# Kernel optimization log

Measured on AMD Instinct MI355X. Metric: run time of the kernel, lower is better.

The kernel has to match this reference:

```python
import jax, jax.numpy as jnp
import numpy as np

N_NODES = 50000
N_EDGES = 50000  # number of hyperedges
NNZ = 800000
IN_C, HID_C, OUT_C = 256, 128, 64


def _glorot(key, shape):
    lim = float(np.sqrt(6.0 / (shape[0] + shape[1])))
    return jax.random.uniform(key, shape, jnp.float32, -lim, lim)


def setup_inputs() -> dict:
    key = jax.random.key(0)
    ks = jax.random.split(key, 8)
    x = jax.random.normal(ks[0], (N_NODES, IN_C), jnp.float32)
    node_idx = jax.random.randint(ks[1], (NNZ,), 0, N_NODES)
    edge_idx = jax.random.randint(ks[2], (NNZ,), 0, N_EDGES)
    hyperedge_index = jnp.stack([node_idx, edge_idx]).astype(jnp.int64)
    return {
        "x": x,
        "hyperedge_index": hyperedge_index,
        "W1": _glorot(ks[3], (IN_C, HID_C)),
        "b1": jnp.zeros((HID_C,), jnp.float32),
        "W2": _glorot(ks[4], (HID_C, OUT_C)),
        "b2": jnp.zeros((OUT_C,), jnp.float32),
        "Wp": _glorot(ks[5], (OUT_C, OUT_C)),
        "bp": jax.random.normal(ks[6], (OUT_C,), jnp.float32) * 0.01,
    }


def _hypergraph_conv(x, node_idx, edge_idx, W, b):
    # PyG HypergraphConv: out = D^-1 H B H^T (X W) + b
    x = x @ W  # [N, F]
    ones = jnp.ones((node_idx.shape[0],), x.dtype)
    d = jax.ops.segment_sum(ones, node_idx, num_segments=N_NODES)   # node degree
    be = jax.ops.segment_sum(ones, edge_idx, num_segments=N_EDGES)  # hyperedge size
    Dinv = jnp.where(d > 0, 1.0 / d, 0.0)
    Binv = jnp.where(be > 0, 1.0 / be, 0.0)
    # node -> hyperedge aggregation
    m = jax.ops.segment_sum(x[node_idx], edge_idx, num_segments=N_EDGES) * Binv[:, None]
    # hyperedge -> node aggregation
    out = jax.ops.segment_sum(m[edge_idx], node_idx, num_segments=N_NODES) * Dinv[:, None]
    return out + b


def reference(x, hyperedge_index, W1, b1, W2, b2, Wp, bp):
    node_idx = hyperedge_index[0]
    edge_idx = hyperedge_index[1]
    h = jax.nn.relu(_hypergraph_conv(x, node_idx, edge_idx, W1, b1))
    features_1 = h
    h = jax.nn.relu(_hypergraph_conv(h, node_idx, edge_idx, W2, b2))
    features_2 = h
    z = h @ Wp + bp
    return (z, features_1, features_2)
```

## Files before the change

kernel.cpp:

```cpp
#include <hip/hip_runtime.h>


typedef unsigned short u16;
typedef unsigned int   u32;
typedef _Float16 f16;
typedef __attribute__((ext_vector_type(8))) short short8;
typedef __attribute__((ext_vector_type(8))) _Float16 half8;
typedef __attribute__((ext_vector_type(4))) float f32x4;

static const int BCAP = 3072;

__device__ __forceinline__ float bf2f(u16 u) {
    return __builtin_bit_cast(float, (u32)u << 16);
}
__device__ __forceinline__ u16 f2bf(float f) {
    u32 b = __builtin_bit_cast(u32, f);
    b += 0x7FFFu + ((b >> 16) & 1u);
    return (u16)(b >> 16);
}

__global__ __launch_bounds__(64) void detect_idx_kernel(const int* __restrict__ hidx,
                                                        int* __restrict__ flag)
{
    __shared__ int nz;
    if (threadIdx.x == 0) nz = 0;
    __syncthreads();
    if (hidx[2 * threadIdx.x + 1] != 0) atomicAdd(&nz, 1);
    __syncthreads();
    if (threadIdx.x == 0) *flag = (nz == 0) ? 1 : 0;
}

__global__ __launch_bounds__(256) void wsplit_kernel(
    const float* __restrict__ W, u16* __restrict__ out, int K, int N)
{
    int idx = blockIdx.x * 256 + threadIdx.x;
    int total = (K >> 6) * N * 72;
    if (idx >= total) return;
    int kp = idx % 72;
    int rest = idx / 72;
    int n = rest % N;
    int c = rest / N;
    float v = 0.f;
    if (kp < 64) v = W[(size_t)(c * 64 + kp) * N + n];
    u16 h = f2bf(v);
    u16 l = f2bf(v - bf2f(h));
    size_t base = (size_t)c * (2 * (size_t)N * 72);
    out[base + (size_t)n * 72 + kp] = h;
    out[base + (size_t)N * 72 + (size_t)n * 72 + kp] = l;
}

__global__ __launch_bounds__(256) void bin_scatter_kernel(
    const int* __restrict__ hidx, const int* __restrict__ flag,
    int* __restrict__ curEb, int* __restrict__ curNb,
    u32* __restrict__ tmpE, u32* __restrict__ tmpN,
    int nnz, int nNodes, int nEdges)
{
    __shared__ int histE[400], histN[400];
    int t = threadIdx.x;
    const int nbE = (nEdges + 127) >> 7, nbN = (nNodes + 127) >> 7;
    for (int b = t; b < 400; b += 256) { histE[b] = 0; histN[b] = 0; }
    __syncthreads();
    int st = (*flag) ? 2 : 1;
    size_t eoff = (size_t)nnz * st;
    int i0 = blockIdx.x * 4096;
    int e_[16], n_[16]; int rE[16], rN[16];
    #pragma unroll
    for (int k = 0; k < 16; ++k) {
        int i = i0 + k * 256 + t;
        int n = -1, e = 0;
        if (i < nnz) {
            n = hidx[(size_t)i * st];
            e = hidx[eoff + (size_t)i * st];
            if (!((u32)n < (u32)nNodes && (u32)e < (u32)nEdges)) n = -1;
        }
        n_[k] = n; e_[k] = e;
        if (n >= 0) {
            rE[k] = atomicAdd(&histE[e >> 7], 1);
            rN[k] = atomicAdd(&histN[n >> 7], 1);
        }
    }
    __syncthreads();
    for (int b = t; b < nbE; b += 256) { int c = histE[b]; if (c) histE[b] = atomicAdd(&curEb[b], c); }
    for (int b = t; b < nbN; b += 256) { int c = histN[b]; if (c) histN[b] = atomicAdd(&curNb[b], c); }
    __syncthreads();
    #pragma unroll
    for (int k = 0; k < 16; ++k) {
        if (n_[k] >= 0) {
            int e = e_[k], n = n_[k];
            int lpE = histE[e >> 7] + rE[k];
            int lpN = histN[n >> 7] + rN[k];
            if (lpE < BCAP) tmpE[(size_t)(e >> 7) * BCAP + lpE] = ((u32)(e & 127) << 16) | (u32)n;
            if (lpN < BCAP) tmpN[(size_t)(n >> 7) * BCAP + lpN] = ((u32)(n & 127) << 16) | (u32)e;
        }
    }
}

__global__ __launch_bounds__(64) void bkt_scan_kernel(
    const int* __restrict__ curE, const int* __restrict__ curN,
    int* __restrict__ baseE, int* __restrict__ baseN, int nbE, int nbN)
{
    const int* cur; int* base; int nb;
    if (blockIdx.x == 0) { cur = curE; base = baseE; nb = nbE; }
    else                 { cur = curN; base = baseN; nb = nbN; }
    int lane = threadIdx.x;
    int carry = 0;
    for (int c0 = 0; c0 < nb; c0 += 64) {
        int i = c0 + lane;
        int v = (i < nb) ? cur[i] : 0;
        int orig = v;
        for (int o = 1; o < 64; o <<= 1) { int u = __shfl_up(v, o, 64); if (lane >= o) v += u; }
        if (i < nb) base[i] = carry + v - orig;
        carry += __shfl(v, 63, 64);
    }
    if (lane == 0) base[nb] = carry;
}

__global__ __launch_bounds__(256) void bin_build_kernel(
    const u32* __restrict__ tmpE, const u32* __restrict__ tmpN,
    const int* __restrict__ baseE, const int* __restrict__ baseN,
    int* __restrict__ deg_e, int* __restrict__ offs_e, float* __restrict__ binv, u16* __restrict__ adj_e,
    int* __restrict__ deg_n, int* __restrict__ offs_n, float* __restrict__ dinv, u16* __restrict__ adj_n,
    int nE, int nN, int nbE)
{
    __shared__ u32 buf[4096];
    __shared__ int lcnt[128], lpre[128], lcur[128];
    int b = blockIdx.x;
    const u32* tmp; const int* base; int* deg; int* offs; float* inv; u16* adj; int n, tb;
    if (b < nbE) { tmp=tmpE; base=baseE; deg=deg_e; offs=offs_e; inv=binv; adj=adj_e; n=nE; tb=b; }
    else         { tmp=tmpN; base=baseN; deg=deg_n; offs=offs_n; inv=dinv; adj=adj_n; n=nN; tb=b-nbE; }
    int t = threadIdx.x;
    int g0 = tb << 7;
    int gbase = base[tb];
    int cnt = base[tb + 1] - gbase;
    int avail = cnt < BCAP ? cnt : BCAP;
    size_t tbase = (size_t)tb * BCAP;
    if (t < 128) lcnt[t] = 0;
    __syncthreads();
    for (int j = t; j < avail; j += 256) atomicAdd(&lcnt[tmp[tbase + j] >> 16], 1);
    __syncthreads();
    if (t < 64) {
        int a0 = lcnt[2 * t], a1 = lcnt[2 * t + 1];
        int ps = a0 + a1, v = ps;
        for (int o = 1; o < 64; o <<= 1) { int u = __shfl_up(v, o, 64); if (t >= o) v += u; }
        int excl = v - ps;
        lpre[2 * t] = excl; lpre[2 * t + 1] = excl + a0;
    }
    __syncthreads();
    if (t < 128) {
        int id = g0 + t;
        if (id < n) {
            int d = lcnt[t];
            deg[id]  = d;
            offs[id] = gbase + lpre[t];
            inv[id]  = d > 0 ? 1.0f / (float)d : 0.0f;
        }
        lcur[t] = lpre[t];
    }
    __syncthreads();
    if (avail <= 0) return;
    for (int j = t; j < avail; j += 256) {
        u32 v = tmp[tbase + j];
        int pos = atomicAdd(&lcur[v >> 16], 1);
        buf[pos] = v & 0xFFFFu;
    }
    __syncthreads();
    for (int j = t; j < avail; j += 256) adj[gbase + j] = (u16)buf[j];
}

template<int C, bool FINAL>
__global__ __launch_bounds__(256) void gather_kernel(
    const f16* __restrict__ src, const u16* __restrict__ adj,
    const int* __restrict__ offs, const int* __restrict__ deg,
    const float* __restrict__ inv, const float* __restrict__ bias,
    void* __restrict__ dstv, int nRows)
{
    constexpr int LANES = C / 8;
    constexpr int ROWS  = 256 / LANES;
    int t = threadIdx.x;
    int row = blockIdx.x * ROWS + t / LANES;
    if (row >= nRows) return;
    int c = (t % LANES) * 8;
    const f16* sp = src + c;
    int j = offs[row], e = j + deg[row];
    float a0[8], a1[8], a2[8], a3[8];
    #pragma unroll
    for (int q = 0; q < 8; ++q) { a0[q] = 0.f; a1[q] = 0.f; a2[q] = 0.f; a3[q] = 0.f; }
    for (; j + 4 <= e; j += 4) {
        int s0 = adj[j], s1 = adj[j + 1], s2 = adj[j + 2], s3 = adj[j + 3];
        const half8 v0 = *(const half8*)(sp + (size_t)s0 * C);
        const half8 v1 = *(const half8*)(sp + (size_t)s1 * C);
        const half8 v2 = *(const half8*)(sp + (size_t)s2 * C);
        const half8 v3 = *(const half8*)(sp + (size_t)s3 * C);
        #pragma unroll
        for (int q = 0; q < 8; ++q) {
            a0[q] += (float)v0[q]; a1[q] += (float)v1[q];
            a2[q] += (float)v2[q]; a3[q] += (float)v3[q];
        }
    }
    for (; j < e; ++j) {
        int s0 = adj[j];
        const half8 v0 = *(const half8*)(sp + (size_t)s0 * C);
        #pragma unroll
        for (int q = 0; q < 8; ++q) a0[q] += (float)v0[q];
    }
    float scv = inv[row];
    float r[8];
    #pragma unroll
    for (int q = 0; q < 8; ++q) r[q] = ((a0[q] + a1[q]) + (a2[q] + a3[q])) * scv;
    if constexpr (FINAL) {
        float* dst = (float*)dstv;
        size_t o = (size_t)row * C + c;
        const float4 b0 = *(const float4*)(bias + c);
        const float4 b1 = *(const float4*)(bias + c + 4);
        float4 o0, o1;
        o0.x = fmaxf(r[0] + b0.x, 0.0f); o0.y = fmaxf(r[1] + b0.y, 0.0f);
        o0.z = fmaxf(r[2] + b0.z, 0.0f); o0.w = fmaxf(r[3] + b0.w, 0.0f);
        o1.x = fmaxf(r[4] + b1.x, 0.0f); o1.y = fmaxf(r[5] + b1.y, 0.0f);
        o1.z = fmaxf(r[6] + b1.z, 0.0f); o1.w = fmaxf(r[7] + b1.w, 0.0f);
        *(float4*)(dst + o)     = o0;
        *(float4*)(dst + o + 4) = o1;
    } else {
        f16* dst = (f16*)dstv;
        half8 ov;
        #pragma unroll
        for (int q = 0; q < 8; ++q) ov[q] = (f16)r[q];
        *(half8*)(dst + (size_t)row * C + c) = ov;
    }
}

__device__ __forceinline__ void split8(const float* __restrict__ p, short8& hi, short8& lo) {
    #pragma unroll
    for (int j = 0; j < 8; ++j) {
        float v = p[j];
        u16 h = f2bf(v);
        hi[j] = (short)h;
        lo[j] = (short)f2bf(v - bf2f(h));
    }
}

template<int K, int N, bool BIAS, bool OUTF16>
__global__ __launch_bounds__(512) void gemm_mfma_kernel(
    const float* __restrict__ A, const u16* __restrict__ Bsp,
    const float* __restrict__ bias, void* __restrict__ C_, int M)
{
    constexpr int KP = 72;
    constexpr int CHUNK = 2 * N * KP;
    constexpr int SC = (K == 256) ? 1 : (K / 64);
    constexpr int NT = N / 16;
    constexpr int NTW = NT / 2;
    __shared__ alignas(16) u16 Bbuf[SC * CHUNK];
    const int tid = threadIdx.x;
    const int wave = tid >> 6, lane = tid & 63;
    const int mg = wave >> 1, nh = wave & 1;
    const int row0 = blockIdx.x * 64 + mg * 16;
    const int lr = lane & 15;
    const int kq = (lane >> 4) * 8;
    const int nt0 = nh * NTW;
    const bool v = row0 < M;
    f32x4 acc[NTW];
    #pragma unroll
    for (int i = 0; i < NTW; ++i) acc[i] = (f32x4){0.f, 0.f, 0.f, 0.f};
    const float* Ap = A + (size_t)(row0 + lr) * K + kq;

    constexpr int CALLS = SC * CHUNK / 512;
    for (int ko = 0; ko < K; ko += SC * 64) {
        const u16* src = Bsp + (size_t)(ko >> 6) * CHUNK;
        if (ko) __syncthreads();
        #pragma unroll
        for (int c = 0; c < (CALLS + 7) / 8; ++c) {
            int call = c * 8 + wave;
            if (call < CALLS) {
                int u = call * 64 + lane;
                *(float4*)(&Bbuf[(size_t)u * 8]) = *(const float4*)(src + (size_t)u * 8);
            }
        }
        __syncthreads();
        if (v) {
            #pragma unroll
            for (int kc = 0; kc < SC; ++kc) {
                #pragma unroll
                for (int k0 = 0; k0 < 64; k0 += 32) {
                    short8 ah, al;
                    split8(Ap + ko + kc * 64 + k0, ah, al);
                    #pragma unroll
                    for (int f = 0; f < NTW; ++f) {
                        const int col = (nt0 + f) * 16 + lr;
                        const int bo = kc * CHUNK + col * KP + k0 + kq;
                        const short8 bh = *(const short8*)(&Bbuf[bo]);
                        const short8 bl = *(const short8*)(&Bbuf[bo + N * KP]);
                        acc[f] = __builtin_amdgcn_mfma_f32_16x16x32_bf16(ah, bh, acc[f], 0, 0, 0);
                        acc[f] = __builtin_amdgcn_mfma_f32_16x16x32_bf16(al, bh, acc[f], 0, 0, 0);
                        acc[f] = __builtin_amdgcn_mfma_f32_16x16x32_bf16(ah, bl, acc[f], 0, 0, 0);
                    }
                }
            }
        }
    }
    if (!v) return;
    const int orow = row0 + (lane >> 4) * 4;
    #pragma unroll
    for (int f = 0; f < NTW; ++f) {
        const int col = (nt0 + f) * 16 + lr;
        float bv = 0.0f;
        if constexpr (BIAS) bv = bias[col];
        #pragma unroll
        for (int j = 0; j < 4; ++j) {
            float vv = acc[f][j] + bv;
            if constexpr (OUTF16) ((f16*)C_)[(size_t)(orow + j) * N + col] = (f16)vv;
            else                  ((float*)C_)[(size_t)(orow + j) * N + col] = vv;
        }
    }
}

extern "C" void kernel_launch(void* const* d_in, const int* in_sizes, int n_in,
                              void* d_out, int out_size, void* d_ws, size_t ws_size,
                              hipStream_t stream)
{
    (void)n_in; (void)out_size; (void)ws_size;
    const float* x  = (const float*)d_in[0];
    const int* hidx = (const int*)d_in[1];
    const float* W1 = (const float*)d_in[2];
    const float* b1 = (const float*)d_in[3];
    const float* W2 = (const float*)d_in[4];
    const float* b2 = (const float*)d_in[5];
    const float* Wp = (const float*)d_in[6];
    const float* bp = (const float*)d_in[7];
    float* out = (float*)d_out;

    const int nnz    = in_sizes[1] / 2;
    const int nNodes = in_sizes[0] / 256;
    const int nEdges = 50000;

    char* w = (char*)d_ws;
    const size_t SEG = 200192;
    int*   deg_e  = (int*)(w + 0 * SEG);
    int*   deg_n  = (int*)(w + 1 * SEG);
    int*   offs_e = (int*)(w + 2 * SEG);
    int*   offs_n = (int*)(w + 3 * SEG);
    float* binv   = (float*)(w + 4 * SEG);
    float* dinv   = (float*)(w + 5 * SEG);
    int*   flag   = (int*)(w + 6 * SEG);
    int*   curEb  = (int*)(w + 6 * SEG + 256);
    int*   curNb  = (int*)(w + 6 * SEG + 2304);
    int*   baseE  = (int*)(w + 6 * SEG + 4352);
    int*   baseN  = (int*)(w + 6 * SEG + 6400);
    char* p = w + 6 * SEG + 8448;
    u16* adj_e = (u16*)p;  p += (size_t)nnz * 2;
    u16* adj_n = (u16*)p;  p += (size_t)nnz * 2;
    f16* h0  = (f16*)p;
    f16* m1  = (f16*)(p + (size_t)nNodes * 128 * 2);
    f16* h1w = h0;
    f16* m2  = (f16*)((char*)h0 + (size_t)nNodes * 64 * 2);
    u16* w1sp = (u16*)(p + 2 * (size_t)nNodes * 128 * 2);
    u16* w2sp = w1sp + 4 * 18432;
    u16* wpsp = w2sp + 2 * 9216;

    const int nbE = (nEdges + 127) >> 7;
    const int nbN = (nNodes + 127) >> 7;
    u32* tmpE = (u32*)m1;
    u32* tmpN = tmpE + (size_t)nbE * BCAP;

    const size_t F1OFF = (size_t)nNodes * 64;
    const size_t F2OFF = F1OFF + (size_t)nNodes * 128;

    hipMemsetAsync(w + 6 * SEG + 256, 0, 4096, stream);
    detect_idx_kernel<<<1, 64, 0, stream>>>(hidx, flag);
    wsplit_kernel<<<(4 * 128 * 72 + 255) / 256, 256, 0, stream>>>(W1, w1sp, 256, 128);
    wsplit_kernel<<<(2 * 64 * 72 + 255) / 256, 256, 0, stream>>>(W2, w2sp, 128, 64);
    wsplit_kernel<<<(1 * 64 * 72 + 255) / 256, 256, 0, stream>>>(Wp, wpsp, 64, 64);
    bin_scatter_kernel<<<(nnz + 4095) / 4096, 256, 0, stream>>>(
        hidx, flag, curEb, curNb, tmpE, tmpN, nnz, nNodes, nEdges);
    bkt_scan_kernel<<<2, 64, 0, stream>>>(curEb, curNb, baseE, baseN, nbE, nbN);
    bin_build_kernel<<<nbE + nbN, 256, 0, stream>>>(
        tmpE, tmpN, baseE, baseN,
        deg_e, offs_e, binv, adj_e,
        deg_n, offs_n, dinv, adj_n,
        nEdges, nNodes, nbE);

    const int gg = (nNodes + 63) / 64;

    gemm_mfma_kernel<256, 128, false, true><<<gg, 512, 0, stream>>>(x, w1sp, nullptr, h0, nNodes);
    gather_kernel<128, false><<<(nEdges + 15) / 16, 256, 0, stream>>>(
        h0, adj_e, offs_e, deg_e, binv, nullptr, m1, nEdges);
    gather_kernel<128, true><<<(nNodes + 15) / 16, 256, 0, stream>>>(
        m1, adj_n, offs_n, deg_n, dinv, b1, out + F1OFF, nNodes);

    gemm_mfma_kernel<128, 64, false, true><<<gg, 512, 0, stream>>>(
        out + F1OFF, w2sp, nullptr, h1w, nNodes);
    gather_kernel<64, false><<<(nEdges + 31) / 32, 256, 0, stream>>>(
        h1w, adj_e, offs_e, deg_e, binv, nullptr, m2, nEdges);
    gather_kernel<64, true><<<(nNodes + 31) / 32, 256, 0, stream>>>(
        m2, adj_n, offs_n, deg_n, dinv, b2, out + F2OFF, nNodes);

    gemm_mfma_kernel<64, 64, true, false><<<gg, 512, 0, stream>>>(
        out + F2OFF, wpsp, bp, out, nNodes);
}
```

Baseline: 289.2 us.

## Store gather sources in column-plane layout and use persistent 1024-thread GEMM

GEMM outputs are now written as column planes (16 or 8 halfs wide), and gather kernels each handle one plane, so a block's random row reads stay inside a smaller working set that fits in cache better. The GEMM becomes persistent with 1024 threads and loads the whole split weight matrix into shared memory once per block. Index-format detection is folded into bin_scatter via a ballot, and the three weight-split kernels are merged into one launch. The risks are that 16-byte random reads per row are less efficient than full-row reads, and that the larger LDS footprint lowers occupancy.

Result: slower. 328.6 us (+13.6%).

```diff
diff --git a/kernel.cpp b/kernel.cpp
--- a/kernel.cpp
+++ b/kernel.cpp
@@ -19,25 +19,11 @@
     return (u16)(b >> 16);
 }
 
-__global__ __launch_bounds__(64) void detect_idx_kernel(const int* __restrict__ hidx,
-                                                        int* __restrict__ flag)
-{
-    __shared__ int nz;
-    if (threadIdx.x == 0) nz = 0;
-    __syncthreads();
-    if (hidx[2 * threadIdx.x + 1] != 0) atomicAdd(&nz, 1);
-    __syncthreads();
-    if (threadIdx.x == 0) *flag = (nz == 0) ? 1 : 0;
-}
-
-__global__ __launch_bounds__(256) void wsplit_kernel(
-    const float* __restrict__ W, u16* __restrict__ out, int K, int N)
-{
-    int idx = blockIdx.x * 256 + threadIdx.x;
-    int total = (K >> 6) * N * 72;
-    if (idx >= total) return;
-    int kp = idx % 72;
-    int rest = idx / 72;
+__device__ __forceinline__ void wsplit_one(const float* __restrict__ W, u16* __restrict__ out,
+                                           int K, int N, int local)
+{
+    int kp = local % 72;
+    int rest = local / 72;
     int n = rest % N;
     int c = rest / N;
     float v = 0.f;
@@ -49,18 +35,36 @@
     out[base + (size_t)N * 72 + (size_t)n * 72 + kp] = l;
 }
 
+__global__ __launch_bounds__(256) void wsplit_all_kernel(
+    const float* __restrict__ W1, const float* __restrict__ W2, const float* __restrict__ Wp,
+    u16* __restrict__ w1sp, u16* __restrict__ w2sp, u16* __restrict__ wpsp)
+{
+    const int T1 = 4 * 128 * 72;
+    const int T2 = 2 * 64 * 72;
+    const int T3 = 1 * 64 * 72;
+    int idx = blockIdx.x * 256 + threadIdx.x;
+    if (idx < T1)                 wsplit_one(W1, w1sp, 256, 128, idx);
+    else if (idx < T1 + T2)       wsplit_one(W2, w2sp, 128, 64, idx - T1);
+    else if (idx < T1 + T2 + T3)  wsplit_one(Wp, wpsp, 64, 64, idx - T1 - T2);
+}
+
 __global__ __launch_bounds__(256) void bin_scatter_kernel(
-    const int* __restrict__ hidx, const int* __restrict__ flag,
+    const int* __restrict__ hidx,
     int* __restrict__ curEb, int* __restrict__ curNb,
     u32* __restrict__ tmpE, u32* __restrict__ tmpN,
     int nnz, int nNodes, int nEdges)
 {
     __shared__ int histE[400], histN[400];
+    __shared__ int s_st;
     int t = threadIdx.x;
     const int nbE = (nEdges + 127) >> 7, nbN = (nNodes + 127) >> 7;
     for (int b = t; b < 400; b += 256) { histE[b] = 0; histN[b] = 0; }
-    __syncthreads();
-    int st = (*flag) ? 2 : 1;
+    if (t < 64) {
+        unsigned long long m = __ballot(hidx[2 * t + 1] != 0);
+        if (t == 0) s_st = (m == 0ull) ? 2 : 1;
+    }
+    __syncthreads();
+    int st = s_st;
     size_t eoff = (size_t)nnz * st;
     int i0 = blockIdx.x * 4096;
     int e_[16], n_[16]; int rE[16], rN[16];
@@ -167,30 +171,32 @@
     for (int j = t; j < avail; j += 256) adj[gbase + j] = (u16)buf[j];
 }
 
-template<int C, bool FINAL>
-__global__ __launch_bounds__(256) void gather_kernel(
+template<int SW, bool FINAL, int C>
+__global__ __launch_bounds__(256) void gather_slice_kernel(
     const f16* __restrict__ src, const u16* __restrict__ adj,
     const int* __restrict__ offs, const int* __restrict__ deg,
     const float* __restrict__ inv, const float* __restrict__ bias,
-    void* __restrict__ dstv, int nRows)
-{
-    constexpr int LANES = C / 8;
-    constexpr int ROWS  = 256 / LANES;
+    void* __restrict__ dstv, int nRows, int nSrcRows)
+{
+    constexpr int TPR = SW / 8;
+    constexpr int RPB = 256 / TPR;
     int t = threadIdx.x;
-    int row = blockIdx.x * ROWS + t / LANES;
-    if (row >= nRows) return;
-    int c = (t % LANES) * 8;
-    const f16* sp = src + c;
-    int j = offs[row], e = j + deg[row];
+    int plane = blockIdx.x & 7;
+    int chunk = blockIdx.x >> 3;
+    int r = chunk * RPB + t / TPR;
+    if (r >= nRows) return;
+    int sub = (TPR == 2) ? (t & 1) : 0;
+    const f16* sp = src + (size_t)plane * nSrcRows * SW + sub * 8;
+    int j = offs[r], e = j + deg[r];
     float a0[8], a1[8], a2[8], a3[8];
     #pragma unroll
     for (int q = 0; q < 8; ++q) { a0[q] = 0.f; a1[q] = 0.f; a2[q] = 0.f; a3[q] = 0.f; }
     for (; j + 4 <= e; j += 4) {
         int s0 = adj[j], s1 = adj[j + 1], s2 = adj[j + 2], s3 = adj[j + 3];
-        const half8 v0 = *(const half8*)(sp + (size_t)s0 * C);
-        const half8 v1 = *(const half8*)(sp + (size_t)s1 * C);
-        const half8 v2 = *(const half8*)(sp + (size_t)s2 * C);
-        const half8 v3 = *(const half8*)(sp + (size_t)s3 * C);
+        const half8 v0 = *(const half8*)(sp + (size_t)s0 * SW);
+        const half8 v1 = *(const half8*)(sp + (size_t)s1 * SW);
+        const half8 v2 = *(const half8*)(sp + (size_t)s2 * SW);
+        const half8 v3 = *(const half8*)(sp + (size_t)s3 * SW);
         #pragma unroll
         for (int q = 0; q < 8; ++q) {
             a0[q] += (float)v0[q]; a1[q] += (float)v1[q];
@@ -199,32 +205,33 @@
     }
     for (; j < e; ++j) {
         int s0 = adj[j];
-        const half8 v0 = *(const half8*)(sp + (size_t)s0 * C);
+        const half8 v0 = *(const half8*)(sp + (size_t)s0 * SW);
         #pragma unroll
         for (int q = 0; q < 8; ++q) a0[q] += (float)v0[q];
     }
-    float scv = inv[row];
-    float r[8];
-    #pragma unroll
-    for (int q = 0; q < 8; ++q) r[q] = ((a0[q] + a1[q]) + (a2[q] + a3[q])) * scv;
+    float scv = inv[r];
+    float rr[8];
+    #pragma unroll
+    for (int q = 0; q < 8; ++q) rr[q] = ((a0[q] + a1[q]) + (a2[q] + a3[q])) * scv;
     if constexpr (FINAL) {
         float* dst = (float*)dstv;
-        size_t o = (size_t)row * C + c;
-        const float4 b0 = *(const float4*)(bias + c);
-        const float4 b1 = *(const float4*)(bias + c + 4);
+        size_t o = (size_t)r * C + plane * SW + sub * 8;
+        const float* bp = bias + plane * SW + sub * 8;
+        const float4 b0 = *(const float4*)(bp);
+        const float4 b1 = *(const float4*)(bp + 4);
         float4 o0, o1;
-        o0.x = fmaxf(r[0] + b0.x, 0.0f); o0.y = fmaxf(r[1] + b0.y, 0.0f);
-        o0.z = fmaxf(r[2] + b0.z, 0.0f); o0.w = fmaxf(r[3] + b0.w, 0.0f);
-        o1.x = fmaxf(r[4] + b1.x, 0.0f); o1.y = fmaxf(r[5] + b1.y, 0.0f);
-        o1.z = fmaxf(r[6] + b1.z, 0.0f); o1.w = fmaxf(r[7] + b1.w, 0.0f);
+        o0.x = fmaxf(rr[0] + b0.x, 0.0f); o0.y = fmaxf(rr[1] + b0.y, 0.0f);
+        o0.z = fmaxf(rr[2] + b0.z, 0.0f); o0.w = fmaxf(rr[3] + b0.w, 0.0f);
+        o1.x = fmaxf(rr[4] + b1.x, 0.0f); o1.y = fmaxf(rr[5] + b1.y, 0.0f);
+        o1.z = fmaxf(rr[6] + b1.z, 0.0f); o1.w = fmaxf(rr[7] + b1.w, 0.0f);
         *(float4*)(dst + o)     = o0;
         *(float4*)(dst + o + 4) = o1;
     } else {
         f16* dst = (f16*)dstv;
         half8 ov;
         #pragma unroll
-        for (int q = 0; q < 8; ++q) ov[q] = (f16)r[q];
-        *(half8*)(dst + (size_t)row * C + c) = ov;
+        for (int q = 0; q < 8; ++q) ov[q] = (f16)rr[q];
+        *(half8*)(dst + (size_t)plane * nRows * SW + (size_t)r * SW + sub * 8) = ov;
     }
 }
 
@@ -238,76 +245,69 @@
     }
 }
 
-template<int K, int N, bool BIAS, bool OUTF16>
-__global__ __launch_bounds__(512) void gemm_mfma_kernel(
+template<int K, int N, bool BIAS, int OUT>
+__global__ __launch_bounds__(1024) void gemm_mfma_kernel(
     const float* __restrict__ A, const u16* __restrict__ Bsp,
     const float* __restrict__ bias, void* __restrict__ C_, int M)
 {
     constexpr int KP = 72;
+    constexpr int NCH = K / 64;
     constexpr int CHUNK = 2 * N * KP;
-    constexpr int SC = (K == 256) ? 1 : (K / 64);
-    constexpr int NT = N / 16;
-    constexpr int NTW = NT / 2;
-    __shared__ alignas(16) u16 Bbuf[SC * CHUNK];
+    constexpr int NTW = N / 32;
+    __shared__ alignas(16) u16 Bbuf[NCH * CHUNK];
     const int tid = threadIdx.x;
+    constexpr int U = NCH * CHUNK / 8;
+    for (int u = tid; u < U; u += 1024)
+        *(float4*)(&Bbuf[(size_t)u * 8]) = *(const float4*)(Bsp + (size_t)u * 8);
+    __syncthreads();
     const int wave = tid >> 6, lane = tid & 63;
     const int mg = wave >> 1, nh = wave & 1;
-    const int row0 = blockIdx.x * 64 + mg * 16;
-    const int lr = lane & 15;
-    const int kq = (lane >> 4) * 8;
+    const int lr = lane & 15, kq = (lane >> 4) * 8;
     const int nt0 = nh * NTW;
-    const bool v = row0 < M;
-    f32x4 acc[NTW];
-    #pragma unroll
-    for (int i = 0; i < NTW; ++i) acc[i] = (f32x4){0.f, 0.f, 0.f, 0.f};
-    const float* Ap = A + (size_t)(row0 + lr) * K + kq;
-
-    constexpr int CALLS = SC * CHUNK / 512;
-    for (int ko = 0; ko < K; ko += SC * 64) {
-        const u16* src = Bsp + (size_t)(ko >> 6) * CHUNK;
-        if (ko) __syncthreads();
-        #pragma unroll
-        for (int c = 0; c < (CALLS + 7) / 8; ++c) {
-            int call = c * 8 + wave;
-            if (call < CALLS) {
-                int u = call * 64 + lane;
-                *(float4*)(&Bbuf[(size_t)u * 8]) = *(const float4*)(src + (size_t)u * 8);
-            }
-        }
-        __syncthreads();
-        if (v) {
+    const int MT = (M + 127) >> 7;
+    for (int tile = blockIdx.x; tile < MT; tile += gridDim.x) {
+        const int row0 = tile * 128 + mg * 16;
+        if (row0 >= M) continue;
+        f32x4 acc[NTW];
+        #pragma unroll
+        for (int i = 0; i < NTW; ++i) acc[i] = (f32x4){0.f, 0.f, 0.f, 0.f};
+        const float* Ap = A + (size_t)(row0 + lr) * K + kq;
+        #pragma unroll
+        for (int c = 0; c < NCH; ++c) {
             #pragma unroll
-            for (int kc = 0; kc < SC; ++kc) {
+            for (int k0 = 0; k0 < 64; k0 += 32) {
+                short8 ah, al;
+                split8(Ap + c * 64 + k0, ah, al);
                 #pragma unroll
-                for (int k0 = 0; k0 < 64; k0 += 32) {
-                    short8 ah, al;
-                    split8(Ap + ko + kc * 64 + k0, ah, al);
-                    #pragma unroll
-                    for (int f = 0; f < NTW; ++f) {
-                        const int col = (nt0 + f) * 16 + lr;
-                        const int bo = kc * CHUNK + col * KP + k0 + kq;
-                        const short8 bh = *(const short8*)(&Bbuf[bo]);
-                        const short8 bl = *(const short8*)(&Bbuf[bo + N * KP]);
-                        acc[f] = __builtin_amdgcn_mfma_f32_16x16x32_bf16(ah, bh, acc[f], 0, 0, 0);
-                        acc[f] = __builtin_amdgcn_mfma_f32_16x16x32_bf16(al, bh, acc[f], 0, 0, 0);
-                        acc[f] = __builtin_amdgcn_mfma_f32_16x16x32_bf16(ah, bl, acc[f], 0, 0, 0);
-                    }
+                for (int f = 0; f < NTW; ++f) {
+                    const int col = (nt0 + f) * 16 + lr;
+                    const int bo = c * CHUNK + col * KP + k0 + kq;
+                    const short8 bh = *(const short8*)(&Bbuf[bo]);
+                    const short8 bl = *(const short8*)(&Bbuf[bo + N * KP]);
+                    acc[f] = __builtin_amdgcn_mfma_f32_16x16x32_bf16(ah, bh, acc[f], 0, 0, 0);
+                    acc[f] = __builtin_amdgcn_mfma_f32_16x16x32_bf16(al, bh, acc[f], 0, 0, 0);
+                    acc[f] = __builtin_amdgcn_mfma_f32_16x16x32_bf16(ah, bl, acc[f], 0, 0, 0);
                 }
             }
         }
-    }
-    if (!v) return;
-    const int orow = row0 + (lane >> 4) * 4;
-    #pragma unroll
-    for (int f = 0; f < NTW; ++f) {
-        const int col = (nt0 + f) * 16 + lr;
-        float bv = 0.0f;
-        if constexpr (BIAS) bv = bias[col];
-        #pragma unroll
-        for (int j = 0; j < 4; ++j) {
-            float vv = acc[f][j] + bv;
-            if constexpr (OUTF16) ((f16*)C_)[(size_t)(orow + j) * N + col] = (f16)vv;
-            else                  ((float*)C_)[(size_t)(orow + j) * N + col] = vv;
+        const int orow = row0 + (lane >> 4) * 4;
+        #pragma unroll
+        for (int f = 0; f < NTW; ++f) {
+            const int col = (nt0 + f) * 16 + lr;
+            float bv = 0.0f;
+            if constexpr (BIAS) bv = bias[col];
+            #pragma unroll
+            for (int j = 0; j < 4; ++j) {
+                float vv = acc[f][j] + bv;
+                if constexpr (OUT == 0) {
+                    ((float*)C_)[(size_t)(orow + j) * N + col] = vv;
+                } else if constexpr (OUT == 1) {
+                    ((f16*)C_)[((size_t)(nt0 + f) * M + (orow + j)) * 16 + lr] = (f16)vv;
+                } else {
+                    const int plane = (nt0 + f) * 2 + (lr >> 3);
+                    ((f16*)C_)[((size_t)plane * M + (orow + j)) * 8 + (lr & 7)] = (f16)vv;
+                }
+            }
         }
     }
 }
@@ -339,7 +339,6 @@
     int*   offs_n = (int*)(w + 3 * SEG);
     float* binv   = (float*)(w + 4 * SEG);
     float* dinv   = (float*)(w + 5 * SEG);
-    int*   flag   = (int*)(w + 6 * SEG);
     int*   curEb  = (int*)(w + 6 * SEG + 256);
     int*   curNb  = (int*)(w + 6 * SEG + 2304);
     int*   baseE  = (int*)(w + 6 * SEG + 4352);
@@ -364,12 +363,10 @@
     const size_t F2OFF = F1OFF + (size_t)nNodes * 128;
 
     hipMemsetAsync(w + 6 * SEG + 256, 0, 4096, stream);
-    detect_idx_kernel<<<1, 64, 0, stream>>>(hidx, flag);
-    wsplit_kernel<<<(4 * 128 * 72 + 255) / 256, 256, 0, stream>>>(W1, w1sp, 256, 128);
-    wsplit_kernel<<<(2 * 64 * 72 + 255) / 256, 256, 0, stream>>>(W2, w2sp, 128, 64);
-    wsplit_kernel<<<(1 * 64 * 72 + 255) / 256, 256, 0, stream>>>(Wp, wpsp, 64, 64);
+    wsplit_all_kernel<<<(4*128*72 + 2*64*72 + 1*64*72 + 255) / 256, 256, 0, stream>>>(
+        W1, W2, Wp, w1sp, w2sp, wpsp);
     bin_scatter_kernel<<<(nnz + 4095) / 4096, 256, 0, stream>>>(
-        hidx, flag, curEb, curNb, tmpE, tmpN, nnz, nNodes, nEdges);
+        hidx, curEb, curNb, tmpE, tmpN, nnz, nNodes, nEdges);
     bkt_scan_kernel<<<2, 64, 0, stream>>>(curEb, curNb, baseE, baseN, nbE, nbN);
     bin_build_kernel<<<nbE + nbN, 256, 0, stream>>>(
         tmpE, tmpN, baseE, baseN,
@@ -377,21 +374,19 @@
         deg_n, offs_n, dinv, adj_n,
         nEdges, nNodes, nbE);
 
-    const int gg = (nNodes + 63) / 64;
-
-    gemm_mfma_kernel<256, 128, false, true><<<gg, 512, 0, stream>>>(x, w1sp, nullptr, h0, nNodes);
-    gather_kernel<128, false><<<(nEdges + 15) / 16, 256, 0, stream>>>(
-        h0, adj_e, offs_e, deg_e, binv, nullptr, m1, nEdges);
-    gather_kernel<128, true><<<(nNodes + 15) / 16, 256, 0, stream>>>(
-        m1, adj_n, offs_n, deg_n, dinv, b1, out + F1OFF, nNodes);
-
-    gemm_mfma_kernel<128, 64, false, true><<<gg, 512, 0, stream>>>(
+    gemm_mfma_kernel<256, 128, false, 1><<<256, 1024, 0, stream>>>(x, w1sp, nullptr, h0, nNodes);
+    gather_slice_kernel<16, false, 128><<<((nEdges + 127) / 128) * 8, 256, 0, stream>>>(
+        h0, adj_e, offs_e, deg_e, binv, nullptr, m1, nEdges, nNodes);
+    gather_slice_kernel<16, true, 128><<<((nNodes + 127) / 128) * 8, 256, 0, stream>>>(
+        m1, adj_n, offs_n, deg_n, dinv, b1, out + F1OFF, nNodes, nEdges);
+
+    gemm_mfma_kernel<128, 64, false, 2><<<391, 1024, 0, stream>>>(
         out + F1OFF, w2sp, nullptr, h1w, nNodes);
-    gather_kernel<64, false><<<(nEdges + 31) / 32, 256, 0, stream>>>(
-        h1w, adj_e, offs_e, deg_e, binv, nullptr, m2, nEdges);
-    gather_kernel<64, true><<<(nNodes + 31) / 32, 256, 0, stream>>>(
-        m2, adj_n, offs_n, deg_n, dinv, b2, out + F2OFF, nNodes);
-
-    gemm_mfma_kernel<64, 64, true, false><<<gg, 512, 0, stream>>>(
+    gather_slice_kernel<8, false, 64><<<((nEdges + 255) / 256) * 8, 256, 0, stream>>>(
+        h1w, adj_e, offs_e, deg_e, binv, nullptr, m2, nEdges, nNodes);
+    gather_slice_kernel<8, true, 64><<<((nNodes + 255) / 256) * 8, 256, 0, stream>>>(
+        m2, adj_n, offs_n, deg_n, dinv, b2, out + F2OFF, nNodes, nEdges);
+
+    gemm_mfma_kernel<64, 64, true, 0><<<391, 1024, 0, stream>>>(
         out + F2OFF, wpsp, bp, out, nNodes);
 }
```
